# Kernel tuning notes

Hardware: AMD Instinct MI355X
Metric: run time of the kernel (lower is better)

Reference implementation:

```python
import jax, jax.numpy as jnp
import numpy as np

B, N, D = 8, 4096, 256
E = 32768
H, C = 4, 64  # heads, per-head dim (hid_dim=256 // heads=4)
NEG_SLOPE = 0.2


def layernorm(x, g, b, eps=1e-5):
    m = jnp.mean(x, axis=-1, keepdims=True)
    v = jnp.var(x, axis=-1, keepdims=True)
    return (x - m) * jax.lax.rsqrt(v + eps) * g + b


def setup_inputs() -> dict:
    key = jax.random.key(0)
    ks = jax.random.split(key, 12)
    def glorot(k, shape):
        lim = np.sqrt(6.0 / (shape[-2] + shape[-1]))
        return jax.random.uniform(k, shape, jnp.float32, -lim, lim)
    return {
        "x": jax.random.normal(ks[0], (B, N, D), jnp.float32),
        "edge_index": jax.random.randint(ks[1], (2, E), 0, N, jnp.int32),
        "W_K": glorot(ks[2], (H * C, D)), "b_K": jnp.zeros((H * C,), jnp.float32),
        "W_V": glorot(ks[3], (H * C, D)), "b_V": jnp.zeros((H * C,), jnp.float32),
        "att_r": glorot(ks[4], (1, H, C)),
        "ln0_g": jnp.ones((H * C,), jnp.float32), "ln0_b": jnp.zeros((H * C,), jnp.float32),
        "ln1_g": jnp.ones((H * C,), jnp.float32), "ln1_b": jnp.zeros((H * C,), jnp.float32),
        "W1": glorot(ks[5], (H * C, H * C)), "b1": jnp.zeros((H * C,), jnp.float32),
        "W2": glorot(ks[6], (H * C, H * C)), "b2": jnp.zeros((H * C,), jnp.float32),
    }


def reference(x, edge_index, W_K, b_K, W_V, b_V, att_r, ln0_g, ln0_b, ln1_g, ln1_b, W1, b1, W2, b2):
    Bq, Nq = x.shape[0], x.shape[1]
    S = Nq  # number of destination segments (fixed for jit)
    src, dst = edge_index[0], edge_index[1]
    # projections -> [B, N, H, C]
    xK = (jnp.einsum('bnd,hd->bnh', x, W_K) + b_K).reshape(Bq, Nq, H, C)
    xV = (jnp.einsum('bnd,hd->bnh', x, W_V) + b_V).reshape(Bq, Nq, H, C)
    # per-node attention logits [B, N, H]
    alpha = jnp.sum(xK * att_r[None], axis=-1)
    # gather to edges, leaky-relu, segment softmax over dst
    a = alpha[:, src]  # [B, E, H]
    a = jnp.where(a >= 0, a, NEG_SLOPE * a)
    a_t = jnp.transpose(a, (1, 0, 2))  # [E, B, H]
    seg_max = jax.ops.segment_max(a_t, dst, num_segments=S)
    seg_max = jnp.where(jnp.isfinite(seg_max), seg_max, 0.0)
    ex = jnp.exp(a_t - seg_max[dst])
    den = jax.ops.segment_sum(ex, dst, num_segments=S)
    w = ex / (den[dst] + 1e-16)  # [E, B, H]
    # weighted scatter-add of values
    v = jnp.transpose(xV[:, src], (1, 0, 2, 3)) * w[..., None]  # [E, B, H, C]
    agg = jax.ops.segment_sum(v, dst, num_segments=S)  # [S, B, H, C]
    out = jnp.transpose(agg, (1, 0, 2, 3)) + att_r[None]  # [B, S, H, C]
    out = out.reshape(Bq, S, H * C)
    out = layernorm(out, ln0_g, ln0_b)
    # rFF: 2-layer MLP, Normalization='None', dropout=0
    h = jax.nn.relu(jnp.einsum('bsd,ed->bse', out, W1) + b1)
    rff = jnp.einsum('bse,fe->bsf', h, W2) + b2
    out = layernorm(out + jax.nn.relu(rff), ln1_g, ln1_b)
    return out
```

## Files before the change

### kernel.cpp

```cpp
#include <hip/hip_runtime.h>
#include <hip/hip_bf16.h>
#include <cstdint>
#include <cstddef>

#define B_   8
#define N_   4096
#define E_   32768
#define ROWS_ 32768
#define NEGSLOPE_ 0.2f
#define NEG_INF_ (-3.402823e38f)

typedef __attribute__((ext_vector_type(8))) __bf16 bf16x8;
typedef __attribute__((ext_vector_type(4))) float  f32x4;

__device__ __forceinline__ float lrelu(float v) { return v >= 0.f ? v : NEGSLOPE_ * v; }

__device__ __forceinline__ float bf2f(ushort u) {
    union { uint32_t i; float f; } c; c.i = ((uint32_t)u) << 16; return c.f;
}
__device__ __forceinline__ ushort f2bf(float f) {
    __hip_bfloat16 h = __float2bfloat16(f);
    return *reinterpret_cast<ushort*>(&h);
}

__device__ __forceinline__ float4 wred_max4(float4 v) {
#pragma unroll
    for (int o = 32; o >= 1; o >>= 1) {
        v.x = fmaxf(v.x, __shfl_xor(v.x, o));
        v.y = fmaxf(v.y, __shfl_xor(v.y, o));
        v.z = fmaxf(v.z, __shfl_xor(v.z, o));
        v.w = fmaxf(v.w, __shfl_xor(v.w, o));
    }
    return v;
}
__device__ __forceinline__ float4 wred_sum4(float4 v) {
#pragma unroll
    for (int o = 32; o >= 1; o >>= 1) {
        v.x += __shfl_xor(v.x, o);
        v.y += __shfl_xor(v.y, o);
        v.z += __shfl_xor(v.z, o);
        v.w += __shfl_xor(v.w, o);
    }
    return v;
}

__global__ void k_prep_u(const float* __restrict__ W_K, const float* __restrict__ b_K,
                         const float* __restrict__ att_r,
                         float* __restrict__ u, float* __restrict__ cvec) {
    int h = blockIdx.x;
    int d = threadIdx.x;
    float s = 0.f;
#pragma unroll 8
    for (int c = 0; c < 64; ++c)
        s += W_K[(size_t)(h*64 + c)*256 + d] * att_r[h*64 + c];
    u[h*256 + d] = s;
    if (d == 0) {
        float cs = 0.f;
        for (int c = 0; c < 64; ++c) cs += b_K[h*64 + c] * att_r[h*64 + c];
        cvec[h] = cs;
    }
}

__global__ void k_cvtW(const float* __restrict__ W_V, const float* __restrict__ W1,
                       const float* __restrict__ W2,
                       ushort* __restrict__ WVb, ushort* __restrict__ W1b,
                       ushort* __restrict__ W2b) {
    int i = blockIdx.x * 1024 + threadIdx.x * 4;
    if (blockIdx.y == 1) {
        int n = i >> 8, c = (i & 255) >> 2;
        const float* s = W1 + (size_t)n*256 + c;
        ushort4 o;
        o.x = f2bf(s[0]);
        o.y = f2bf(s[64]);
        o.z = f2bf(s[128]);
        o.w = f2bf(s[192]);
        *(ushort4*)&W1b[i] = o;
    } else {
        const float* s = (blockIdx.y == 0) ? W_V : W2;
        ushort* d      = (blockIdx.y == 0) ? WVb : W2b;
        float4 v = *(const float4*)&s[i];
        ushort4 o; o.x = f2bf(v.x); o.y = f2bf(v.y); o.z = f2bf(v.z); o.w = f2bf(v.w);
        *(ushort4*)&d[i] = o;
    }
}

__global__ void k_alpha(const float* __restrict__ x, const float* __restrict__ u,
                        const float* __restrict__ cvec, float* __restrict__ alpha,
                        ushort* __restrict__ xb) {
    int wave = threadIdx.x >> 6, lane = threadIdx.x & 63;
    size_t row = (size_t)blockIdx.x * 4 + wave;
    const float4* x4 = (const float4*)(x + row*256);
    float4 xv = x4[lane];
    ushort4 xw; xw.x = f2bf(xv.x); xw.y = f2bf(xv.y); xw.z = f2bf(xv.z); xw.w = f2bf(xv.w);
    *(ushort4*)&xb[row*256 + lane*4] = xw;

    const float4* u4 = (const float4*)u;
    float res[4];
#pragma unroll
    for (int h = 0; h < 4; ++h) {
        float4 uv = u4[h*64 + lane];
        float p = xv.x*uv.x + xv.y*uv.y + xv.z*uv.z + xv.w*uv.w;
#pragma unroll
        for (int o = 32; o >= 1; o >>= 1) p += __shfl_xor(p, o);
        res[h] = p;
    }
    if (lane == 0) {
        float4 cv = *(const float4*)cvec;
        float4 o;
        o.x = lrelu(res[0] + cv.x);
        o.y = lrelu(res[1] + cv.y);
        o.z = lrelu(res[2] + cv.z);
        o.w = lrelu(res[3] + cv.w);
        *(float4*)(alpha + row*4) = o;
    }
}

__global__ void k_hist(const int* __restrict__ ei, int* __restrict__ counts) {
    int e = blockIdx.x * 256 + threadIdx.x;
    if (e < E_) atomicAdd(&counts[ei[E_ + e]], 1);
}

__global__ void k_scan(const int* __restrict__ counts, int* __restrict__ offsets) {
    __shared__ int tot[256];
    int t = threadIdx.x;
    int local[16];
    int s = 0;
#pragma unroll
    for (int i = 0; i < 16; ++i) { local[i] = s; s += counts[t*16 + i]; }
    tot[t] = s;
    __syncthreads();
    for (int d = 1; d < 256; d <<= 1) {
        int v = (t >= d) ? tot[t - d] : 0;
        __syncthreads();
        tot[t] += v;
        __syncthreads();
    }
    int base = (t == 0) ? 0 : tot[t - 1];
#pragma unroll
    for (int i = 0; i < 16; ++i) offsets[t*16 + i] = base + local[i];
    if (t == 255) offsets[4096] = tot[255];
}

__global__ void k_fill(const int* __restrict__ ei, const int* __restrict__ offsets,
                       int* __restrict__ cursor, int* __restrict__ bucket_src) {
    int e = blockIdx.x * 256 + threadIdx.x;
    if (e >= E_) return;
    int d = ei[E_ + e], srcn = ei[e];
    int pos = atomicAdd(&cursor[d], 1);
    bucket_src[offsets[d] + pos] = srcn;
}

__global__ __launch_bounds__(256) void k_agg_ln0(
        const float* __restrict__ alpha, const ushort* __restrict__ xVb,
        const int* __restrict__ offsets, const int* __restrict__ bucket_src,
        const float* __restrict__ att_r,
        const float* __restrict__ g0, const float* __restrict__ b0,
        ushort* __restrict__ out0b) {
    __shared__ float4 s_w4[4][64];
    int t = threadIdx.x, wv = t >> 6, lane = t & 63;
    int gp = blockIdx.x * 4 + wv;
    int n = gp >> 3, b = gp & 7;
    int beg = offsets[n], end = offsets[n + 1];
    size_t brow = (size_t)b * N_;

    float4 m4   = make_float4(NEG_INF_, NEG_INF_, NEG_INF_, NEG_INF_);
    float4 den4 = make_float4(0.f, 0.f, 0.f, 0.f);
    float4 acc4 = make_float4(0.f, 0.f, 0.f, 0.f);

    for (int chunk = beg; chunk < end; chunk += 64) {
        int cnt = min(64, end - chunk);
        int my_src = (lane < cnt) ? bucket_src[chunk + lane] : 0;
        float4 a4 = make_float4(NEG_INF_, NEG_INF_, NEG_INF_, NEG_INF_);
        if (lane < cnt) a4 = *(const float4*)&alpha[(brow + my_src)*4];

        float4 mc = wred_max4(a4);
        float4 mn;
        mn.x = fmaxf(m4.x, mc.x); mn.y = fmaxf(m4.y, mc.y);
        mn.z = fmaxf(m4.z, mc.z); mn.w = fmaxf(m4.w, mc.w);
        float4 ex;
        ex.x = __expf(a4.x - mn.x); ex.y = __expf(a4.y - mn.y);
        ex.z = __expf(a4.z - mn.z); ex.w = __expf(a4.w - mn.w);
        float4 ss = wred_sum4(ex);
        float4 r;
        r.x = __expf(m4.x - mn.x); r.y = __expf(m4.y - mn.y);
        r.z = __expf(m4.z - mn.z); r.w = __expf(m4.w - mn.w);
        den4.x = den4.x * r.x + ss.x; den4.y = den4.y * r.y + ss.y;
        den4.z = den4.z * r.z + ss.z; den4.w = den4.w * r.w + ss.w;
        acc4.x *= r.x; acc4.y *= r.y; acc4.z *= r.z; acc4.w *= r.w;
        m4 = mn;
        s_w4[wv][lane] = ex;

        for (int e = 0; e < cnt; e += 4) {
#pragma unroll
            for (int k = 0; k < 4; ++k) {
                int srcn = __shfl(my_src, e + k);
                float4 w4 = s_w4[wv][e + k];
                ushort4 v = *(const ushort4*)&xVb[(brow + srcn)*256 + lane*4];
                acc4.x += w4.x * bf2f(v.x);
                acc4.y += w4.y * bf2f(v.y);
                acc4.z += w4.z * bf2f(v.z);
                acc4.w += w4.w * bf2f(v.w);
            }
        }
    }

    float4 o4;
    o4.x = acc4.x / (den4.x + 1e-16f) + att_r[lane];
    o4.y = acc4.y / (den4.y + 1e-16f) + att_r[64 + lane];
    o4.z = acc4.z / (den4.z + 1e-16f) + att_r[128 + lane];
    o4.w = acc4.w / (den4.w + 1e-16f) + att_r[192 + lane];

    float s1 = o4.x + o4.y + o4.z + o4.w;
    float s2 = o4.x*o4.x + o4.y*o4.y + o4.z*o4.z + o4.w*o4.w;
#pragma unroll
    for (int o = 32; o >= 1; o >>= 1) { s1 += __shfl_xor(s1, o); s2 += __shfl_xor(s2, o); }
    float mean = s1 * (1.f/256.f);
    float inv = rsqrtf(s2 * (1.f/256.f) - mean*mean + 1e-5f);

    ushort4 st;
    st.x = f2bf((o4.x - mean) * inv * g0[lane]       + b0[lane]);
    st.y = f2bf((o4.y - mean) * inv * g0[64 + lane]  + b0[64 + lane]);
    st.z = f2bf((o4.z - mean) * inv * g0[128 + lane] + b0[128 + lane]);
    st.w = f2bf((o4.w - mean) * inv * g0[192 + lane] + b0[192 + lane]);
    *(ushort4*)&out0b[(brow + n)*256 + lane*4] = st;
}

__global__ __launch_bounds__(256) void k_gemm0(const ushort* __restrict__ A,
                                               const ushort* __restrict__ Bw,
                                               const float* __restrict__ bias,
                                               ushort* ob) {
    __shared__ __align__(16) ushort As[64*32];
    __shared__ __align__(16) ushort Bs[256*32];

    int t = threadIdx.x;
    int w = t >> 6, lane = t & 63;
    int fr = lane & 15, fg = lane >> 4;
    size_t m0 = (size_t)blockIdx.x * 64;

    int srow = t >> 2;
    int schunk = (t & 3) ^ (srow & 3);
    const ushort* gA  = A  + (m0 + srow)*256 + schunk*8;
    const ushort* gB0 = Bw + (size_t)srow*256 + schunk*8;

    int chnk = (fg ^ (fr & 3)) * 8;

    f32x4 acc[4][4];
#pragma unroll
    for (int mt = 0; mt < 4; ++mt)
#pragma unroll
        for (int nt = 0; nt < 4; ++nt) acc[mt][nt] = (f32x4){0.f, 0.f, 0.f, 0.f};

    for (int ks = 0; ks < 8; ++ks) {
        int k0 = ks * 32;
        __builtin_amdgcn_global_load_lds(
            (const __attribute__((address_space(1))) void*)(gA + k0),
            (__attribute__((address_space(3))) void*)(&As[t*8]), 16, 0, 0);
#pragma unroll
        for (int rr = 0; rr < 4; ++rr)
            __builtin_amdgcn_global_load_lds(
                (const __attribute__((address_space(1))) void*)(gB0 + rr*16384 + k0),
                (__attribute__((address_space(3))) void*)(&Bs[rr*2048 + t*8]), 16, 0, 0);
        __syncthreads();

        bf16x8 a[4], b[4];
#pragma unroll
        for (int mt = 0; mt < 4; ++mt)
            a[mt] = *(const bf16x8*)&As[(mt*16 + fr)*32 + chnk];
#pragma unroll
        for (int nt = 0; nt < 4; ++nt)
            b[nt] = *(const bf16x8*)&Bs[(w*64 + nt*16 + fr)*32 + chnk];
#pragma unroll
        for (int mt = 0; mt < 4; ++mt)
#pragma unroll
            for (int nt = 0; nt < 4; ++nt)
                acc[mt][nt] = __builtin_amdgcn_mfma_f32_16x16x32_bf16(
                    a[mt], b[nt], acc[mt][nt], 0, 0, 0);
        __syncthreads();
    }

    float biasv[4];
#pragma unroll
    for (int nt = 0; nt < 4; ++nt) biasv[nt] = bias[w*64 + fr + nt*16];
#pragma unroll
    for (int mt = 0; mt < 4; ++mt)
#pragma unroll
        for (int j = 0; j < 4; ++j) {
            int row = mt*16 + fg*4 + j;
#pragma unroll
            for (int nt = 0; nt < 4; ++nt) {
                float v = acc[mt][nt][j] + biasv[nt];
                int col = ((fr + nt*16) << 2) | w;
                ob[(m0 + row)*256 + col] = f2bf(v);
            }
        }
}

__global__ __launch_bounds__(256) void k_mlp(const ushort* __restrict__ A,
                                             const ushort* __restrict__ W1b,
                                             const float* __restrict__ b1,
                                             const ushort* __restrict__ W2b,
                                             const float* __restrict__ b2,
                                             const float* __restrict__ g,
                                             const float* __restrict__ bvec,
                                             float* __restrict__ out) {
    __shared__ __align__(16) ushort As[8*32*32];
    __shared__ __align__(16) ushort Bs[256*32];
    __shared__ __align__(16) ushort Hs[32*256];
    __shared__ float2 red[32][4];

    int t = threadIdx.x;
    int w = t >> 6, lane = t & 63;
    int fr = lane & 15, fg = lane >> 4;
    size_t m0 = (size_t)blockIdx.x * 32;

    int srow = t >> 2;
    int schunk = (t & 3) ^ (srow & 3);
    const ushort* gA  = A   + (m0 + srow)*256 + schunk*8;
    const ushort* gW1 = W1b + (size_t)srow*256 + schunk*8;
    const ushort* gW2 = W2b + (size_t)srow*256 + schunk*8;

    int chnk = (fg ^ (fr & 3)) * 8;

    f32x4 acc1[2][4];
#pragma unroll
    for (int mt = 0; mt < 2; ++mt)
#pragma unroll
        for (int nt = 0; nt < 4; ++nt) acc1[mt][nt] = (f32x4){0.f, 0.f, 0.f, 0.f};

    for (int ks = 0; ks < 8; ++ks) {
        int k0 = ks * 32;
        if (t < 128)
            __builtin_amdgcn_global_load_lds(
                (const __attribute__((address_space(1))) void*)(gA + k0),
                (__attribute__((address_space(3))) void*)(&As[ks*1024 + t*8]), 16, 0, 0);
#pragma unroll
        for (int rr = 0; rr < 4; ++rr)
            __builtin_amdgcn_global_load_lds(
                (const __attribute__((address_space(1))) void*)(gW1 + rr*16384 + k0),
                (__attribute__((address_space(3))) void*)(&Bs[rr*2048 + t*8]), 16, 0, 0);
        __syncthreads();

        bf16x8 a[2], b[4];
#pragma unroll
        for (int mt = 0; mt < 2; ++mt)
            a[mt] = *(const bf16x8*)&As[ks*1024 + (mt*16 + fr)*32 + chnk];
#pragma unroll
        for (int nt = 0; nt < 4; ++nt)
            b[nt] = *(const bf16x8*)&Bs[(w*64 + nt*16 + fr)*32 + chnk];
#pragma unroll
        for (int mt = 0; mt < 2; ++mt)
#pragma unroll
            for (int nt = 0; nt < 4; ++nt)
                acc1[mt][nt] = __builtin_amdgcn_mfma_f32_16x16x32_bf16(
                    a[mt], b[nt], acc1[mt][nt], 0, 0, 0);
        __syncthreads();
    }

    int colb = w*64 + fr;
    {
        float b1v[4];
#pragma unroll
        for (int nt = 0; nt < 4; ++nt) b1v[nt] = b1[colb + nt*16];
#pragma unroll
        for (int mt = 0; mt < 2; ++mt)
#pragma unroll
            for (int j = 0; j < 4; ++j) {
                int row = mt*16 + fg*4 + j;
#pragma unroll
                for (int nt = 0; nt < 4; ++nt) {
                    float v = fmaxf(acc1[mt][nt][j] + b1v[nt], 0.f);
                    int byteoff = (row*512 + (colb + nt*16)*2) ^ ((row & 7) << 4);
                    *(ushort*)((char*)Hs + byteoff) = f2bf(v);
                }
            }
    }
    __syncthreads();

    f32x4 acc2[2][4];
#pragma unroll
    for (int mt = 0; mt < 2; ++mt)
#pragma unroll
        for (int nt = 0; nt < 4; ++nt) acc2[mt][nt] = (f32x4){0.f, 0.f, 0.f, 0.f};

    for (int ks = 0; ks < 8; ++ks) {
        int k0 = ks * 32;
#pragma unroll
        for (int rr = 0; rr < 4; ++rr)
            __builtin_amdgcn_global_load_lds(
                (const __attribute__((address_space(1))) void*)(gW2 + rr*16384 + k0),
                (__attribute__((address_space(3))) void*)(&Bs[rr*2048 + t*8]), 16, 0, 0);
        __syncthreads();

        bf16x8 a[2], b[4];
#pragma unroll
        for (int mt = 0; mt < 2; ++mt) {
            int row = mt*16 + fr;
            int byteoff = (row*512 + (k0 + fg*8)*2) ^ ((row & 7) << 4);
            a[mt] = *(const bf16x8*)((char*)Hs + byteoff);
        }
#pragma unroll
        for (int nt = 0; nt < 4; ++nt)
            b[nt] = *(const bf16x8*)&Bs[(w*64 + nt*16 + fr)*32 + chnk];
#pragma unroll
        for (int mt = 0; mt < 2; ++mt)
#pragma unroll
            for (int nt = 0; nt < 4; ++nt)
                acc2[mt][nt] = __builtin_amdgcn_mfma_f32_16x16x32_bf16(
                    a[mt], b[nt], acc2[mt][nt], 0, 0, 0);
        __syncthreads();
    }

    float b2v[4], gv[4], bvv[4];
#pragma unroll
    for (int nt = 0; nt < 4; ++nt) {
        b2v[nt] = b2[colb + nt*16];
        gv[nt]  = g[colb + nt*16];
        bvv[nt] = bvec[colb + nt*16];
    }
#pragma unroll
    for (int mt = 0; mt < 2; ++mt)
#pragma unroll
        for (int j = 0; j < 4; ++j) {
            int row = mt*16 + fg*4 + j;
            float p1 = 0.f, p2 = 0.f;
#pragma unroll
            for (int nt = 0; nt < 4; ++nt) {
                float v = fmaxf(acc2[mt][nt][j] + b2v[nt], 0.f);
                int kp  = ((nt*16 + fr) << 2) | w;
                int ks2 = kp >> 5, off = kp & 31;
                int idx = ks2*1024 + row*32 + ((off >> 3) ^ (row & 3))*8 + (off & 7);
                float y = bf2f(As[idx]) + v;
                acc2[mt][nt][j] = y;
                p1 += y; p2 += y*y;
            }
#pragma unroll
            for (int o = 8; o >= 1; o >>= 1) { p1 += __shfl_xor(p1, o); p2 += __shfl_xor(p2, o); }
            if (fr == 0) red[row][w] = make_float2(p1, p2);
        }
    __syncthreads();
#pragma unroll
    for (int mt = 0; mt < 2; ++mt)
#pragma unroll
        for (int j = 0; j < 4; ++j) {
            int row = mt*16 + fg*4 + j;
            float2 s0 = red[row][0], sA = red[row][1], sB = red[row][2], sC = red[row][3];
            float s = s0.x + sA.x + sB.x + sC.x;
            float q = s0.y + sA.y + sB.y + sC.y;
            float mean = s * (1.f/256.f);
            float inv = rsqrtf(q * (1.f/256.f) - mean*mean + 1e-5f);
#pragma unroll
            for (int nt = 0; nt < 4; ++nt)
                out[(m0 + row)*256 + colb + nt*16] =
                    (acc2[mt][nt][j] - mean) * inv * gv[nt] + bvv[nt];
        }
}

extern "C" void kernel_launch(void* const* d_in, const int* in_sizes, int n_in,
                              void* d_out, int out_size, void* d_ws, size_t ws_size,
                              hipStream_t stream) {
    const float* x     = (const float*)d_in[0];
    const int*   ei    = (const int*)  d_in[1];
    const float* W_K   = (const float*)d_in[2];
    const float* b_K   = (const float*)d_in[3];
    const float* W_V   = (const float*)d_in[4];
    const float* b_V   = (const float*)d_in[5];
    const float* att_r = (const float*)d_in[6];
    const float* ln0_g = (const float*)d_in[7];
    const float* ln0_b = (const float*)d_in[8];
    const float* ln1_g = (const float*)d_in[9];
    const float* ln1_b = (const float*)d_in[10];
    const float* W1    = (const float*)d_in[11];
    const float* b1    = (const float*)d_in[12];
    const float* W2    = (const float*)d_in[13];
    const float* b2    = (const float*)d_in[14];
    float* out = (float*)d_out;

    char* wsb = (char*)d_ws;
    float*  u     = (float*) (wsb);
    float*  cvec  = (float*) (wsb + 4096);
    float*  alpha = (float*) (wsb + 8192);
    ushort* WVb   = (ushort*)(wsb + 532480);
    ushort* W1b   = WVb + 65536;
    ushort* W2b   = W1b + 65536;
    int*    ints  = (int*)  (W2b + 65536);
    int* counts   = ints;
    int* cursor   = ints + 4096;
    int* offsets  = ints + 8192;
    int* bucket   = ints + 12544;
    ushort* bufA  = (ushort*)(wsb + 1114112);
    ushort* bufB  = bufA + 8388608;
    size_t need   = 1114112 + 2ull*16777216;

    if (ws_size < need) return;

    hipMemsetAsync(counts, 0, 8192 * sizeof(int), stream);

    k_prep_u <<<4, 256, 0, stream>>>(W_K, b_K, att_r, u, cvec);
    k_cvtW   <<<dim3(64, 3), 256, 0, stream>>>(W_V, W1, W2, WVb, W1b, W2b);
    k_alpha  <<<ROWS_/4, 256, 0, stream>>>(x, u, cvec, alpha, bufA);
    k_gemm0  <<<ROWS_/64, 256, 0, stream>>>(bufA, WVb, b_V, bufA);
    k_hist   <<<E_/256, 256, 0, stream>>>(ei, counts);
    k_scan   <<<1, 256, 0, stream>>>(counts, offsets);
    k_fill   <<<E_/256, 256, 0, stream>>>(ei, offsets, cursor, bucket);
    k_agg_ln0<<<ROWS_/4, 256, 0, stream>>>(alpha, bufA, offsets, bucket,
                                           att_r, ln0_g, ln0_b, bufB);
    k_mlp    <<<ROWS_/32, 256, 0, stream>>>(bufB, W1b, b1, W2b, b2,
                                            ln1_g, ln1_b, out);
}
```

Baseline: 209.0 us.

## Merge small launches, double-buffer GEMM weight staging, and stage outputs through LDS

Merges weight conversion, u/cvec prep and the dst histogram into one setup kernel, and puts the bucket fill inside the value-projection GEMM kernel as extra blocks. This cuts the launch count from nine to six. The GEMM and MLP kernels now double-buffer weight tiles in LDS so the next K-slice loads while MFMAs run. They also write results through an LDS tile for coalesced 16-byte stores. The aggregation inner loop unrolls by 8 instead of 4, and LDS use per block rises, which may lower occupancy.

```diff
diff --git a/kernel.cpp b/kernel.cpp
--- a/kernel.cpp
+++ b/kernel.cpp
@@ -44,43 +44,51 @@
     return v;
 }
 
-__global__ void k_prep_u(const float* __restrict__ W_K, const float* __restrict__ b_K,
-                         const float* __restrict__ att_r,
-                         float* __restrict__ u, float* __restrict__ cvec) {
-    int h = blockIdx.x;
-    int d = threadIdx.x;
-    float s = 0.f;
+#define GLDS(gp, lp) __builtin_amdgcn_global_load_lds( \
+    (const __attribute__((address_space(1))) void*)(gp), \
+    (__attribute__((address_space(3))) void*)(lp), 16, 0, 0)
+
+__global__ __launch_bounds__(256) void k_setup(
+        const float* __restrict__ W_K, const float* __restrict__ b_K,
+        const float* __restrict__ att_r, float* __restrict__ u,
+        float* __restrict__ cvec,
+        const float* __restrict__ W_V, const float* __restrict__ W1,
+        const float* __restrict__ W2,
+        ushort* __restrict__ WVb, ushort* __restrict__ W1b,
+        ushort* __restrict__ W2b,
+        const int* __restrict__ ei, int* __restrict__ counts) {
+    int bid = blockIdx.x, t = threadIdx.x;
+    if (bid < 192) {
+        int bx = bid & 63, by = bid >> 6;
+        int i = bx * 1024 + t * 4;
+        if (by == 1) {
+            int n = i >> 8, c = (i & 255) >> 2;
+            const float* s = W1 + (size_t)n*256 + c;
+            ushort4 o;
+            o.x = f2bf(s[0]); o.y = f2bf(s[64]); o.z = f2bf(s[128]); o.w = f2bf(s[192]);
+            *(ushort4*)&W1b[i] = o;
+        } else {
+            const float* s = (by == 0) ? W_V : W2;
+            ushort* d      = (by == 0) ? WVb : W2b;
+            float4 v = *(const float4*)&s[i];
+            ushort4 o; o.x = f2bf(v.x); o.y = f2bf(v.y); o.z = f2bf(v.z); o.w = f2bf(v.w);
+            *(ushort4*)&d[i] = o;
+        }
+    } else if (bid < 196) {
+        int h = bid - 192, d = t;
+        float s = 0.f;
 #pragma unroll 8
-    for (int c = 0; c < 64; ++c)
-        s += W_K[(size_t)(h*64 + c)*256 + d] * att_r[h*64 + c];
-    u[h*256 + d] = s;
-    if (d == 0) {
-        float cs = 0.f;
-        for (int c = 0; c < 64; ++c) cs += b_K[h*64 + c] * att_r[h*64 + c];
-        cvec[h] = cs;
-    }
-}
-
-__global__ void k_cvtW(const float* __restrict__ W_V, const float* __restrict__ W1,
-                       const float* __restrict__ W2,
-                       ushort* __restrict__ WVb, ushort* __restrict__ W1b,
-                       ushort* __restrict__ W2b) {
-    int i = blockIdx.x * 1024 + threadIdx.x * 4;
-    if (blockIdx.y == 1) {
-        int n = i >> 8, c = (i & 255) >> 2;
-        const float* s = W1 + (size_t)n*256 + c;
-        ushort4 o;
-        o.x = f2bf(s[0]);
-        o.y = f2bf(s[64]);
-        o.z = f2bf(s[128]);
-        o.w = f2bf(s[192]);
-        *(ushort4*)&W1b[i] = o;
+        for (int c = 0; c < 64; ++c)
+            s += W_K[(size_t)(h*64 + c)*256 + d] * att_r[h*64 + c];
+        u[h*256 + d] = s;
+        if (d == 0) {
+            float cs = 0.f;
+            for (int c = 0; c < 64; ++c) cs += b_K[h*64 + c] * att_r[h*64 + c];
+            cvec[h] = cs;
+        }
     } else {
-        const float* s = (blockIdx.y == 0) ? W_V : W2;
-        ushort* d      = (blockIdx.y == 0) ? WVb : W2b;
-        float4 v = *(const float4*)&s[i];
-        ushort4 o; o.x = f2bf(v.x); o.y = f2bf(v.y); o.z = f2bf(v.z); o.w = f2bf(v.w);
-        *(ushort4*)&d[i] = o;
+        int e = (bid - 196) * 256 + t;
+        if (e < E_) atomicAdd(&counts[ei[E_ + e]], 1);
     }
 }
 
@@ -115,11 +123,6 @@
     }
 }
 
-__global__ void k_hist(const int* __restrict__ ei, int* __restrict__ counts) {
-    int e = blockIdx.x * 256 + threadIdx.x;
-    if (e < E_) atomicAdd(&counts[ei[E_ + e]], 1);
-}
-
 __global__ void k_scan(const int* __restrict__ counts, int* __restrict__ offsets) {
     __shared__ int tot[256];
     int t = threadIdx.x;
@@ -141,13 +144,93 @@
     if (t == 255) offsets[4096] = tot[255];
 }
 
-__global__ void k_fill(const int* __restrict__ ei, const int* __restrict__ offsets,
-                       int* __restrict__ cursor, int* __restrict__ bucket_src) {
-    int e = blockIdx.x * 256 + threadIdx.x;
-    if (e >= E_) return;
-    int d = ei[E_ + e], srcn = ei[e];
-    int pos = atomicAdd(&cursor[d], 1);
-    bucket_src[offsets[d] + pos] = srcn;
+__global__ __launch_bounds__(256) void k_g0f(const ushort* __restrict__ A,
+                                             const ushort* __restrict__ Bw,
+                                             const float* __restrict__ bias,
+                                             ushort* ob,
+                                             const int* __restrict__ ei,
+                                             const int* __restrict__ offsets,
+                                             int* __restrict__ cursor,
+                                             int* __restrict__ bucket) {
+    __shared__ __align__(16) ushort sA[2][2048];
+    __shared__ __align__(16) ushort sB[2][8192];
+    int t = threadIdx.x;
+
+    if (blockIdx.x >= 512) {
+        int e = (blockIdx.x - 512) * 256 + t;
+        if (e < E_) {
+            int d = ei[E_ + e], srcn = ei[e];
+            int pos = atomicAdd(&cursor[d], 1);
+            bucket[offsets[d] + pos] = srcn;
+        }
+        return;
+    }
+
+    int w = t >> 6, lane = t & 63;
+    int fr = lane & 15, fg = lane >> 4;
+    size_t m0 = (size_t)blockIdx.x * 64;
+
+    int srow = t >> 2;
+    int schunk = (t & 3) ^ (srow & 3);
+    const ushort* gA  = A  + (m0 + srow)*256 + schunk*8;
+    const ushort* gB0 = Bw + (size_t)srow*256 + schunk*8;
+    int chnk = (fg ^ (fr & 3)) * 8;
+
+    f32x4 acc[4][4];
+#pragma unroll
+    for (int mt = 0; mt < 4; ++mt)
+#pragma unroll
+        for (int nt = 0; nt < 4; ++nt) acc[mt][nt] = (f32x4){0.f, 0.f, 0.f, 0.f};
+
+    auto STAGE = [&](int buf, int ks) {
+        int k0 = ks * 32;
+        GLDS(gA + k0, &sA[buf][t*8]);
+#pragma unroll
+        for (int rr = 0; rr < 4; ++rr)
+            GLDS(gB0 + rr*16384 + k0, &sB[buf][rr*2048 + t*8]);
+    };
+
+    STAGE(0, 0);
+    __syncthreads();
+    for (int ks = 0; ks < 8; ++ks) {
+        int cur = ks & 1;
+        if (ks < 7) STAGE(cur ^ 1, ks + 1);
+        bf16x8 a[4], b[4];
+#pragma unroll
+        for (int mt = 0; mt < 4; ++mt)
+            a[mt] = *(const bf16x8*)&sA[cur][(mt*16 + fr)*32 + chnk];
+#pragma unroll
+        for (int nt = 0; nt < 4; ++nt)
+            b[nt] = *(const bf16x8*)&sB[cur][(w*64 + nt*16 + fr)*32 + chnk];
+#pragma unroll
+        for (int mt = 0; mt < 4; ++mt)
+#pragma unroll
+            for (int nt = 0; nt < 4; ++nt)
+                acc[mt][nt] = __builtin_amdgcn_mfma_f32_16x16x32_bf16(
+                    a[mt], b[nt], acc[mt][nt], 0, 0, 0);
+        __syncthreads();
+    }
+
+    ushort* tile = &sB[0][0];
+    float biasv[4];
+#pragma unroll
+    for (int nt = 0; nt < 4; ++nt) biasv[nt] = bias[w*64 + fr + nt*16];
+#pragma unroll
+    for (int mt = 0; mt < 4; ++mt)
+#pragma unroll
+        for (int j = 0; j < 4; ++j) {
+            int row = mt*16 + fg*4 + j;
+#pragma unroll
+            for (int nt = 0; nt < 4; ++nt) {
+                float v = acc[mt][nt][j] + biasv[nt];
+                tile[row*256 + (((fr + nt*16) << 2) | w)] = f2bf(v);
+            }
+        }
+    __syncthreads();
+    const int4* ts = (const int4*)tile;
+    int4* td = (int4*)(ob + m0*256);
+#pragma unroll
+    for (int i = 0; i < 8; ++i) td[i*256 + t] = ts[i*256 + t];
 }
 
 __global__ __launch_bounds__(256) void k_agg_ln0(
@@ -190,9 +273,9 @@
         m4 = mn;
         s_w4[wv][lane] = ex;
 
-        for (int e = 0; e < cnt; e += 4) {
-#pragma unroll
-            for (int k = 0; k < 4; ++k) {
+        for (int e = 0; e < cnt; e += 8) {
+#pragma unroll
+            for (int k = 0; k < 8; ++k) {
                 int srcn = __shfl(my_src, e + k);
                 float4 w4 = s_w4[wv][e + k];
                 ushort4 v = *(const ushort4*)&xVb[(brow + srcn)*256 + lane*4];
@@ -225,77 +308,7 @@
     *(ushort4*)&out0b[(brow + n)*256 + lane*4] = st;
 }
 
-__global__ __launch_bounds__(256) void k_gemm0(const ushort* __restrict__ A,
-                                               const ushort* __restrict__ Bw,
-                                               const float* __restrict__ bias,
-                                               ushort* ob) {
-    __shared__ __align__(16) ushort As[64*32];
-    __shared__ __align__(16) ushort Bs[256*32];
-
-    int t = threadIdx.x;
-    int w = t >> 6, lane = t & 63;
-    int fr = lane & 15, fg = lane >> 4;
-    size_t m0 = (size_t)blockIdx.x * 64;
-
-    int srow = t >> 2;
-    int schunk = (t & 3) ^ (srow & 3);
-    const ushort* gA  = A  + (m0 + srow)*256 + schunk*8;
-    const ushort* gB0 = Bw + (size_t)srow*256 + schunk*8;
-
-    int chnk = (fg ^ (fr & 3)) * 8;
-
-    f32x4 acc[4][4];
-#pragma unroll
-    for (int mt = 0; mt < 4; ++mt)
-#pragma unroll
-        for (int nt = 0; nt < 4; ++nt) acc[mt][nt] = (f32x4){0.f, 0.f, 0.f, 0.f};
-
-    for (int ks = 0; ks < 8; ++ks) {
-        int k0 = ks * 32;
-        __builtin_amdgcn_global_load_lds(
-            (const __attribute__((address_space(1))) void*)(gA + k0),
-            (__attribute__((address_space(3))) void*)(&As[t*8]), 16, 0, 0);
-#pragma unroll
-        for (int rr = 0; rr < 4; ++rr)
-            __builtin_amdgcn_global_load_lds(
-                (const __attribute__((address_space(1))) void*)(gB0 + rr*16384 + k0),
-                (__attribute__((address_space(3))) void*)(&Bs[rr*2048 + t*8]), 16, 0, 0);
-        __syncthreads();
-
-        bf16x8 a[4], b[4];
-#pragma unroll
-        for (int mt = 0; mt < 4; ++mt)
-            a[mt] = *(const bf16x8*)&As[(mt*16 + fr)*32 + chnk];
-#pragma unroll
-        for (int nt = 0; nt < 4; ++nt)
-            b[nt] = *(const bf16x8*)&Bs[(w*64 + nt*16 + fr)*32 + chnk];
-#pragma unroll
-        for (int mt = 0; mt < 4; ++mt)
-#pragma unroll
-            for (int nt = 0; nt < 4; ++nt)
-                acc[mt][nt] = __builtin_amdgcn_mfma_f32_16x16x32_bf16(
-                    a[mt], b[nt], acc[mt][nt], 0, 0, 0);
-        __syncthreads();
-    }
-
-    float biasv[4];
-#pragma unroll
-    for (int nt = 0; nt < 4; ++nt) biasv[nt] = bias[w*64 + fr + nt*16];
-#pragma unroll
-    for (int mt = 0; mt < 4; ++mt)
-#pragma unroll
-        for (int j = 0; j < 4; ++j) {
-            int row = mt*16 + fg*4 + j;
-#pragma unroll
-            for (int nt = 0; nt < 4; ++nt) {
-                float v = acc[mt][nt][j] + biasv[nt];
-                int col = ((fr + nt*16) << 2) | w;
-                ob[(m0 + row)*256 + col] = f2bf(v);
-            }
-        }
-}
-
-__global__ __launch_bounds__(256) void k_mlp(const ushort* __restrict__ A,
+__global__ __launch_bounds__(256) void k_mlp(const ushort* __restrict__ Ain,
                                              const ushort* __restrict__ W1b,
                                              const float* __restrict__ b1,
                                              const ushort* __restrict__ W2b,
@@ -303,10 +316,9 @@
                                              const float* __restrict__ g,
                                              const float* __restrict__ bvec,
                                              float* __restrict__ out) {
-    __shared__ __align__(16) ushort As[8*32*32];
-    __shared__ __align__(16) ushort Bs[256*32];
-    __shared__ __align__(16) ushort Hs[32*256];
-    __shared__ float2 red[32][4];
+    __shared__ __align__(16) ushort As[8192];
+    __shared__ __align__(16) ushort Bs[2][8192];
+    __shared__ __align__(16) ushort Hs[8192];
 
     int t = threadIdx.x;
     int w = t >> 6, lane = t & 63;
@@ -315,12 +327,28 @@
 
     int srow = t >> 2;
     int schunk = (t & 3) ^ (srow & 3);
-    const ushort* gA  = A   + (m0 + srow)*256 + schunk*8;
     const ushort* gW1 = W1b + (size_t)srow*256 + schunk*8;
     const ushort* gW2 = W2b + (size_t)srow*256 + schunk*8;
-
     int chnk = (fg ^ (fr & 3)) * 8;
 
+    auto stageW = [&](int buf, const ushort* gW, int ks) {
+        int k0 = ks * 32;
+#pragma unroll
+        for (int rr = 0; rr < 4; ++rr)
+            GLDS(gW + rr*16384 + k0, &Bs[buf][rr*2048 + t*8]);
+    };
+
+    {
+        int row = (t >> 2) & 31, cs = t & 3, sc = cs ^ (row & 3);
+#pragma unroll
+        for (int p = 0; p < 4; ++p) {
+            int ks = p*2 + (t >> 7);
+            GLDS(Ain + (m0 + row)*256 + ks*32 + sc*8, &As[p*2048 + t*8]);
+        }
+    }
+    stageW(0, gW1, 0);
+    __syncthreads();
+
     f32x4 acc1[2][4];
 #pragma unroll
     for (int mt = 0; mt < 2; ++mt)
@@ -328,25 +356,15 @@
         for (int nt = 0; nt < 4; ++nt) acc1[mt][nt] = (f32x4){0.f, 0.f, 0.f, 0.f};
 
     for (int ks = 0; ks < 8; ++ks) {
-        int k0 = ks * 32;
-        if (t < 128)
-            __builtin_amdgcn_global_load_lds(
-                (const __attribute__((address_space(1))) void*)(gA + k0),
-                (__attribute__((address_space(3))) void*)(&As[ks*1024 + t*8]), 16, 0, 0);
-#pragma unroll
-        for (int rr = 0; rr < 4; ++rr)
-            __builtin_amdgcn_global_load_lds(
-                (const __attribute__((address_space(1))) void*)(gW1 + rr*16384 + k0),
-                (__attribute__((address_space(3))) void*)(&Bs[rr*2048 + t*8]), 16, 0, 0);
-        __syncthreads();
-
+        int cur = ks & 1;
+        if (ks < 7) stageW(cur ^ 1, gW1, ks + 1);
         bf16x8 a[2], b[4];
 #pragma unroll
         for (int mt = 0; mt < 2; ++mt)
             a[mt] = *(const bf16x8*)&As[ks*1024 + (mt*16 + fr)*32 + chnk];
 #pragma unroll
         for (int nt = 0; nt < 4; ++nt)
-            b[nt] = *(const bf16x8*)&Bs[(w*64 + nt*16 + fr)*32 + chnk];
+            b[nt] = *(const bf16x8*)&Bs[cur][(w*64 + nt*16 + fr)*32 + chnk];
 #pragma unroll
         for (int mt = 0; mt < 2; ++mt)
 #pragma unroll
@@ -355,6 +373,8 @@
                     a[mt], b[nt], acc1[mt][nt], 0, 0, 0);
         __syncthreads();
     }
+
+    stageW(0, gW2, 0);
 
     int colb = w*64 + fr;
     {
@@ -383,14 +403,9 @@
         for (int nt = 0; nt < 4; ++nt) acc2[mt][nt] = (f32x4){0.f, 0.f, 0.f, 0.f};
 
     for (int ks = 0; ks < 8; ++ks) {
+        int cur = ks & 1;
+        if (ks < 7) stageW(cur ^ 1, gW2, ks + 1);
         int k0 = ks * 32;
-#pragma unroll
-        for (int rr = 0; rr < 4; ++rr)
-            __builtin_amdgcn_global_load_lds(
-                (const __attribute__((address_space(1))) void*)(gW2 + rr*16384 + k0),
-                (__attribute__((address_space(3))) void*)(&Bs[rr*2048 + t*8]), 16, 0, 0);
-        __syncthreads();
-
         bf16x8 a[2], b[4];
 #pragma unroll
         for (int mt = 0; mt < 2; ++mt) {
@@ -400,7 +415,7 @@
         }
 #pragma unroll
         for (int nt = 0; nt < 4; ++nt)
-            b[nt] = *(const bf16x8*)&Bs[(w*64 + nt*16 + fr)*32 + chnk];
+            b[nt] = *(const bf16x8*)&Bs[cur][(w*64 + nt*16 + fr)*32 + chnk];
 #pragma unroll
         for (int mt = 0; mt < 2; ++mt)
 #pragma unroll
@@ -410,6 +425,7 @@
         __syncthreads();
     }
 
+    float2 (*red)[4] = (float2(*)[4])Hs;
     float b2v[4], gv[4], bvv[4];
 #pragma unroll
     for (int nt = 0; nt < 4; ++nt) {
@@ -438,21 +454,28 @@
             if (fr == 0) red[row][w] = make_float2(p1, p2);
         }
     __syncthreads();
+
+    float* tileF = (float*)&Bs[0][0];
 #pragma unroll
     for (int mt = 0; mt < 2; ++mt)
 #pragma unroll
         for (int j = 0; j < 4; ++j) {
             int row = mt*16 + fg*4 + j;
-            float2 s0 = red[row][0], sA = red[row][1], sB = red[row][2], sC = red[row][3];
-            float s = s0.x + sA.x + sB.x + sC.x;
-            float q = s0.y + sA.y + sB.y + sC.y;
+            float2 s0 = red[row][0], sA2 = red[row][1], sB2 = red[row][2], sC = red[row][3];
+            float s = s0.x + sA2.x + sB2.x + sC.x;
+            float q = s0.y + sA2.y + sB2.y + sC.y;
             float mean = s * (1.f/256.f);
             float inv = rsqrtf(q * (1.f/256.f) - mean*mean + 1e-5f);
 #pragma unroll
             for (int nt = 0; nt < 4; ++nt)
-                out[(m0 + row)*256 + colb + nt*16] =
+                tileF[row*256 + colb + nt*16] =
                     (acc2[mt][nt][j] - mean) * inv * gv[nt] + bvv[nt];
         }
+    __syncthreads();
+    const int4* ts = (const int4*)tileF;
+    int4* td = (int4*)(out + m0*256);
+#pragma unroll
+    for (int i = 0; i < 8; ++i) td[i*256 + t] = ts[i*256 + t];
 }
 
 extern "C" void kernel_launch(void* const* d_in, const int* in_sizes, int n_in,
@@ -495,13 +518,12 @@
 
     hipMemsetAsync(counts, 0, 8192 * sizeof(int), stream);
 
-    k_prep_u <<<4, 256, 0, stream>>>(W_K, b_K, att_r, u, cvec);
-    k_cvtW   <<<dim3(64, 3), 256, 0, stream>>>(W_V, W1, W2, WVb, W1b, W2b);
+    k_setup  <<<324, 256, 0, stream>>>(W_K, b_K, att_r, u, cvec,
+                                       W_V, W1, W2, WVb, W1b, W2b, ei, counts);
     k_alpha  <<<ROWS_/4, 256, 0, stream>>>(x, u, cvec, alpha, bufA);
-    k_gemm0  <<<ROWS_/64, 256, 0, stream>>>(bufA, WVb, b_V, bufA);
-    k_hist   <<<E_/256, 256, 0, stream>>>(ei, counts);
     k_scan   <<<1, 256, 0, stream>>>(counts, offsets);
-    k_fill   <<<E_/256, 256, 0, stream>>>(ei, offsets, cursor, bucket);
+    k_g0f    <<<640, 256, 0, stream>>>(bufA, WVb, b_V, bufA,
+                                       ei, offsets, cursor, bucket);
     k_agg_ln0<<<ROWS_/4, 256, 0, stream>>>(alpha, bufA, offsets, bucket,
                                            att_r, ln0_g, ln0_b, bufB);
     k_mlp    <<<ROWS_/32, 256, 0, stream>>>(bufB, W1b, b1, W2b, b2,
```

After: 204.4 us. 2.2% less time.
